# Kernel optimization log

Measured on AMD Instinct MI355X. Metric: run time of the kernel, lower is better.

The kernel has to match this reference:

```python
import jax, jax.numpy as jnp
import numpy as np

T, B, IN, H, OUT = 1024, 128, 6, 1536, 5


def setup_inputs() -> dict:
    key = jax.random.key(0)
    ks = jax.random.split(key, 11)
    s = 1.0 / np.sqrt(H)  # PyTorch cell init range
    u = lambda k, shape: jax.random.uniform(k, shape, jnp.float32, -s, s)
    return {
        "rnn_input": jax.random.normal(ks[0], (T, B, IN), jnp.float32),
        "W_ih0": u(ks[1], (4 * H, IN)),
        "W_hh0": u(ks[2], (4 * H, H)),
        "b_ih0": u(ks[3], (4 * H,)),
        "b_hh0": u(ks[4], (4 * H,)),
        "W_ih1": u(ks[5], (4 * H, H)),
        "W_hh1": u(ks[6], (4 * H, H)),
        "b_ih1": u(ks[7], (4 * H,)),
        "b_hh1": u(ks[8], (4 * H,)),
        "W_lin": u(ks[9], (OUT, H)),
        "b_lin": u(ks[10], (OUT,)),
    }


def _lstm_cell(x, h, c, W_ih, W_hh, b):
    # PyTorch LSTMCell: gates ordered (input, forget, cell, output)
    gates = x @ W_ih.T + h @ W_hh.T + b  # [B, 4H]
    i, f, g, o = jnp.split(gates, 4, axis=-1)
    c_new = jax.nn.sigmoid(f) * c + jax.nn.sigmoid(i) * jnp.tanh(g)
    h_new = jax.nn.sigmoid(o) * jnp.tanh(c_new)
    return h_new, c_new


def reference(rnn_input, W_ih0, W_hh0, b_ih0, b_hh0,
              W_ih1, W_hh1, b_ih1, b_hh1, W_lin, b_lin):
    b0 = b_ih0 + b_hh0
    b1 = b_ih1 + b_hh1
    batch = rnn_input.shape[1]
    h = rnn_input.dtype
    z = jnp.zeros((batch, H), h)

    def step(carry, x_t):
        h0, c0, h1, c1 = carry
        h0, c0 = _lstm_cell(x_t, h0, c0, W_ih0, W_hh0, b0)
        h1, c1 = _lstm_cell(h0, h1, c1, W_ih1, W_hh1, b1)
        return (h0, c0, h1, c1), None

    (h0, c0, h1, c1), _ = jax.lax.scan(step, (z, z, z, z), rnn_input)
    # Module's forward returns only the last-timestep linear output
    return h1 @ W_lin.T + b_lin  # [B, OUT]
```

## Files before the change

### kernel.cpp

```cpp
#include <hip/hip_runtime.h>

#define TSTEPS 1024
#define BATCH  128
#define HDIM   1536
#define NB_L0  96
#define NB_L1  128
#define NBLK   (NB_L0 + NB_L1)
#define K0P    1600
#define K1P    3072

typedef _Float16 f16x8 __attribute__((ext_vector_type(8)));
typedef float    f32x4 __attribute__((ext_vector_type(4)));

#define OFF_C0   0ul
#define OFF_C1   1024ul
#define OFF_H0   4096ul
#define OFF_H1   (OFF_H0 + 4ul*BATCH*HDIM*2)
#define OFF_WP0  (OFF_H1 + 2ul*BATCH*HDIM*2)
#define OFF_WP1  (OFF_WP0 + 96ul*64*K0P*2)
#define OFF_WLP  (OFF_WP1 + 128ul*48*K1P*2)
#define WS_NEED  (OFF_WLP + 16ul*HDIM*2)

#define SM_PARK  98304
#define SM_CST   147456
#define SM_BG    155648
#define SM_BYTES 155904

#define MFMA(a,b,c) __builtin_amdgcn_mfma_f32_16x16x32_f16(a,b,c,0,0,0)
#define LDSBAR()  asm volatile("s_waitcnt lgkmcnt(0)\n\ts_barrier" ::: "memory")
#define WAITVM8() asm volatile("s_waitcnt vmcnt(8)" ::: "memory")
#define WAITVM0() asm volatile("s_waitcnt vmcnt(0)" ::: "memory")

__device__ __forceinline__ float sgf(float x) { return 1.f/(1.f + __expf(-x)); }
__device__ __forceinline__ float thf(float x) { float e = __expf(2.f*x); return 1.f - 2.f/(e+1.f); }

__device__ __forceinline__ void gld16(const _Float16* g, char* lds) {
  __builtin_amdgcn_global_load_lds(
      (const __attribute__((address_space(1))) unsigned int*)g,
      (__attribute__((address_space(3))) unsigned int*)lds, 16, 0, 0);
}

__device__ __forceinline__ void group_bar(unsigned* lines, unsigned target, int tid) {
  __syncthreads();
  if (tid == 0)
    __hip_atomic_fetch_add(lines + (blockIdx.x & 7)*32, 1u,
                           __ATOMIC_RELEASE, __HIP_MEMORY_SCOPE_AGENT);
  if (tid < 8) {
    while (__hip_atomic_load(lines + tid*32, __ATOMIC_RELAXED,
                             __HIP_MEMORY_SCOPE_AGENT) < target)
      __builtin_amdgcn_s_sleep(1);
    __builtin_amdgcn_fence(__ATOMIC_ACQUIRE, "agent");
  }
  __syncthreads();
}

__device__ __forceinline__ void wait_group(unsigned* lines, unsigned target, int tid) {
  if (tid < 8) {
    while (__hip_atomic_load(lines + tid*32, __ATOMIC_RELAXED,
                             __HIP_MEMORY_SCOPE_AGENT) < target)
      __builtin_amdgcn_s_sleep(1);
    __builtin_amdgcn_fence(__ATOMIC_ACQUIRE, "agent");
  }
  __syncthreads();
}

__global__ void convert_weights(const float* __restrict__ Wih0, const float* __restrict__ Whh0,
                                const float* __restrict__ Wih1, const float* __restrict__ Whh1,
                                const float* __restrict__ Wlin,
                                _Float16* __restrict__ Wp0, _Float16* __restrict__ Wp1,
                                _Float16* __restrict__ Wlp) {
  const unsigned N0 = 96u*64u*K0P, N1 = 128u*48u*K1P, N2 = 16u*HDIM;
  const unsigned NT = N0 + N1 + N2;
  for (unsigned i = blockIdx.x*blockDim.x + threadIdx.x; i < NT; i += gridDim.x*blockDim.x) {
    if (i < N0) {
      unsigned blk = i / (64u*K0P), r = i - blk*64u*K0P;
      unsigned p = r / K0P, kk = r - p*K0P;
      unsigned srow = (p>>4)*HDIM + blk*16 + (p&15);
      float v;
      if (kk < 64u) v = (kk < 6u) ? Wih0[srow*6 + kk] : 0.f;
      else          v = Whh0[(size_t)srow*HDIM + (kk-64u)];
      Wp0[i] = (_Float16)v;
    } else if (i < N0 + N1) {
      unsigned ii = i - N0;
      unsigned blk = ii / (48u*K1P), r = ii - blk*48u*K1P;
      unsigned p = r / K1P, kk = r - p*K1P;
      unsigned srow = (p/12u)*HDIM + blk*12 + (p%12u);
      float v = (kk < (unsigned)HDIM) ? Wih1[(size_t)srow*HDIM + kk]
                                      : Whh1[(size_t)srow*HDIM + (kk-HDIM)];
      Wp1[ii] = (_Float16)v;
    } else {
      unsigned ii = i - N0 - N1;
      unsigned rr = ii / HDIM, k = ii - rr*HDIM;
      Wlp[ii] = (_Float16)(rr < 5 ? Wlin[rr*HDIM + k] : 0.f);
    }
  }
}

__global__ __launch_bounds__(256, 1) void lstm_persistent(
    const float* __restrict__ xall,
    const float* __restrict__ bih0, const float* __restrict__ bhh0,
    const float* __restrict__ bih1, const float* __restrict__ bhh1,
    const float* __restrict__ blin,
    const _Float16* __restrict__ Wp0, const _Float16* __restrict__ Wp1,
    const _Float16* __restrict__ Wlp,
    _Float16* __restrict__ h0b, _Float16* __restrict__ h1b,
    unsigned* __restrict__ c0l, unsigned* __restrict__ c1l,
    float* __restrict__ out)
{
  extern __shared__ __align__(16) char smem[];
  char*  park = smem + SM_PARK;
  float* cst  = (float*)(smem + SM_CST);
  float* bg   = (float*)(smem + SM_BG);
  float* gbuf = (float*)smem;

  const int tid = threadIdx.x, bid = blockIdx.x;
  const int wv = tid >> 6, lane = tid & 63, q = lane >> 4, l15 = lane & 15;
  const int BH = BATCH*HDIM;

  int dmaoff[8];
#pragma unroll
  for (int i = 0; i < 8; ++i) {
    int m = wv*32 + i*4 + (lane>>4), w16 = lane & 15;
    int u = (w16 & 8) | ((w16 ^ (m & 7)) & 7);
    dmaoff[i] = m*HDIM + u*8;
  }
  const int uA = wv*4 + q;
  int addrA[8];
#pragma unroll
  for (int mt = 0; mt < 8; ++mt) {
    int m = mt*16 + l15;
    int swz = (uA & 8) | ((uA ^ (m & 7)) & 7);
    addrA[mt] = m*256 + swz*16;
  }

  if (bid < NB_L0) {
    for (int p = tid; p < 64; p += 256) {
      int srow = (p>>4)*HDIM + (bid<<4) + (p&15);
      bg[p] = bih0[srow] + bhh0[srow];
    }
    for (int i = tid; i < BATCH*16; i += 256) cst[i] = 0.f;
    f16x8 bw[13][4];
#pragma unroll
    for (int wi = 0; wi < 13; ++wi)
#pragma unroll
      for (int nt = 0; nt < 4; ++nt)
        bw[wi][nt] = *(const f16x8*)(Wp0 + ((size_t)(bid*64 + nt*16 + l15))*K0P
                                         + (4*wi + wv)*32 + q*8);
    __syncthreads();

#pragma unroll 1
    for (int s = 0; s < TSTEPS; ++s) {
      if (s >= 4) wait_group(c1l, 16u*(unsigned)(s-3), tid);

      const _Float16* h0r = h0b + (size_t)((s+3)&3)*BH;
      _Float16*       h0w = h0b + (size_t)(s&3)*BH;
      const float*    xs  = xall + (size_t)s*BATCH*6;

#pragma unroll
      for (int i = 0; i < 8; ++i)
        gld16(h0r + 64 + dmaoff[i], smem + 32768 + (wv*8+i)*1024);
#pragma unroll
      for (int i = 0; i < 4; ++i) {
        int sidx = i*256 + tid, m = sidx>>3, w8 = sidx&7;
        int u = w8 ^ (m & 7);
        f16x8 v = {0,0,0,0,0,0,0,0};
        if (u == 0) {
#pragma unroll
          for (int j = 0; j < 6; ++j) v[j] = (_Float16)xs[m*6 + j];
        }
        *(f16x8*)(smem + m*256 + w8*16) = v;
      }
#pragma unroll
      for (int i = 0; i < 4; ++i) {
        int sidx = i*256 + tid, m = sidx>>3, w8 = sidx&7;
        int u8 = (w8 ^ (m & 7)) & 7;
        f16x8 hv = *(const f16x8*)(h0r + m*HDIM + u8*8);
        *(f16x8*)(smem + m*256 + (8 + w8)*16) = hv;
      }
      f32x4 acc[8][4];
#pragma unroll
      for (int mt = 0; mt < 8; ++mt)
#pragma unroll
        for (int nt = 0; nt < 4; ++nt) { f32x4 z = {0,0,0,0}; acc[mt][nt] = z; }

#pragma unroll
      for (int wi = 0; wi < 13; ++wi) {
        if (wi == 12)      WAITVM0();
        else if (wi >= 1)  WAITVM8();
        LDSBAR();
        if (wi + 2 < 13) {
          const _Float16* src = h0r + (wi+2)*128 - 64;
          char* dst = smem + ((wi+2)%3)*32768;
#pragma unroll
          for (int i = 0; i < 8; ++i) gld16(src + dmaoff[i], dst + (wv*8+i)*1024);
        }
        if (4*wi + wv < 50) {
          const char* bs = smem + (wi%3)*32768;
#pragma unroll
          for (int mt = 0; mt < 8; ++mt) {
            f16x8 a = *(const f16x8*)(bs + addrA[mt]);
#pragma unroll
            for (int nt = 0; nt < 4; ++nt)
              acc[mt][nt] = MFMA(a, bw[wi][nt], acc[mt][nt]);
          }
        }
      }
      LDSBAR();

#pragma unroll
      for (int r = 0; r < 4; ++r) {
        int nt = (wv + r) & 3;
#pragma unroll
        for (int mt = 0; mt < 8; ++mt) {
          f32x4 av = (nt==0)?acc[mt][0]:(nt==1)?acc[mt][1]:(nt==2)?acc[mt][2]:acc[mt][3];
          float* p = gbuf + (nt*16 + l15)*132 + (mt*16 + q*4);
          if (r == 0) *(f32x4*)p = av;
          else        { f32x4 o = *(const f32x4*)p; *(f32x4*)p = o + av; }
        }
        LDSBAR();
      }
#pragma unroll
      for (int e = 0; e < 8; ++e) {
        int idx = e*256 + tid, m = idx>>4, j = idx&15;
        float gi = gbuf[j*132 + m]        + bg[j];
        float gf = gbuf[(16+j)*132 + m]   + bg[16+j];
        float gg = gbuf[(32+j)*132 + m]   + bg[32+j];
        float go = gbuf[(48+j)*132 + m]   + bg[48+j];
        float co = cst[m*16 + j];
        float cn = sgf(gf)*co + sgf(gi)*thf(gg);
        cst[m*16 + j] = cn;
        h0w[(size_t)m*HDIM + (bid<<4) + j] = (_Float16)(sgf(go)*thf(cn));
      }
      group_bar(c0l, 12u*(unsigned)(s+1), tid);
    }
  } else {
    const int bid1 = bid - NB_L0;
    for (int p = tid; p < 48; p += 256) {
      int srow = (p/12)*HDIM + bid1*12 + (p%12);
      bg[p] = bih1[srow] + bhh1[srow];
    }
    for (int i = tid; i < 64*12; i += 256) cst[i] = 0.f;
    f16x8 bw1[20][3];
#pragma unroll
    for (int wi = 0; wi < 20; ++wi)
#pragma unroll
      for (int nt = 0; nt < 3; ++nt)
        bw1[wi][nt] = *(const f16x8*)(Wp1 + ((size_t)(bid1*48 + nt*16 + l15))*K1P
                                          + (4*wi + wv)*32 + q*8);
    for (int idx = tid; idx < 16*3*64; idx += 256) {
      int cl = idx/192, rem = idx - cl*192, nt = rem>>6, l = rem&63;
      f16x8 v = *(const f16x8*)(Wp1 + ((size_t)(bid1*48 + nt*16 + (l&15)))*K1P
                                    + (80 + cl)*32 + (l>>4)*8);
      *(f16x8*)(park + idx*16) = v;
    }
    __syncthreads();

#pragma unroll 1
    for (int s = 1; s <= TSTEPS; ++s) {
      wait_group(c0l, 12u*(unsigned)s, tid);

      const _Float16* h0r = h0b + (size_t)((s-1)&3)*BH;
      const _Float16* h1r = h1b + (size_t)(s&1)*BH;
      _Float16*       h1w = h1b + (size_t)((s-1)&1)*BH;

#pragma unroll
      for (int i = 0; i < 8; ++i) gld16(h0r +   0 + dmaoff[i], smem +     0 + (wv*8+i)*1024);
#pragma unroll
      for (int i = 0; i < 8; ++i) gld16(h0r + 128 + dmaoff[i], smem + 32768 + (wv*8+i)*1024);
      f32x4 acc[8][3];
#pragma unroll
      for (int mt = 0; mt < 8; ++mt)
#pragma unroll
        for (int nt = 0; nt < 3; ++nt) { f32x4 z = {0,0,0,0}; acc[mt][nt] = z; }

#pragma unroll
      for (int wi = 0; wi < 24; ++wi) {
        if (wi == 23) WAITVM0(); else WAITVM8();
        LDSBAR();
        if (wi + 2 < 24) {
          int wn = wi + 2;
          const _Float16* src = (wn < 12) ? (h0r + wn*128) : (h1r + (wn-12)*128);
          char* dst = smem + (wn%3)*32768;
#pragma unroll
          for (int i = 0; i < 8; ++i) gld16(src + dmaoff[i], dst + (wv*8+i)*1024);
        }
        const char* bs = smem + (wi%3)*32768;
        if (wi < 20) {
#pragma unroll
          for (int mt = 0; mt < 8; ++mt) {
            f16x8 a = *(const f16x8*)(bs + addrA[mt]);
#pragma unroll
            for (int nt = 0; nt < 3; ++nt)
              acc[mt][nt] = MFMA(a, bw1[wi][nt], acc[mt][nt]);
          }
        } else {
          f16x8 p0 = *(const f16x8*)(park + ((((wi-20)*4 + wv)*3 + 0)*64 + lane)*16);
          f16x8 p1 = *(const f16x8*)(park + ((((wi-20)*4 + wv)*3 + 1)*64 + lane)*16);
          f16x8 p2 = *(const f16x8*)(park + ((((wi-20)*4 + wv)*3 + 2)*64 + lane)*16);
#pragma unroll
          for (int mt = 0; mt < 8; ++mt) {
            f16x8 a = *(const f16x8*)(bs + addrA[mt]);
            acc[mt][0] = MFMA(a, p0, acc[mt][0]);
            acc[mt][1] = MFMA(a, p1, acc[mt][1]);
            acc[mt][2] = MFMA(a, p2, acc[mt][2]);
          }
        }
      }
      LDSBAR();

#pragma unroll
      for (int r = 0; r < 4; ++r) {
        int nt = (wv + r) & 3;
        if (nt < 3) {
#pragma unroll
          for (int mt = 0; mt < 8; ++mt) {
            f32x4 av = (nt==0)?acc[mt][0]:(nt==1)?acc[mt][1]:acc[mt][2];
            float* p = gbuf + (nt*16 + l15)*132 + (mt*16 + q*4);
            if (r == 0) *(f32x4*)p = av;
            else        { f32x4 o = *(const f32x4*)p; *(f32x4*)p = o + av; }
          }
        }
        LDSBAR();
      }
#pragma unroll
      for (int e = 0; e < 8; ++e) {
        int idx = e*256 + tid, m = idx>>4, j = idx&15;
        if (j < 12) {
          float gi = gbuf[j*132 + m]        + bg[j];
          float gf = gbuf[(12+j)*132 + m]   + bg[12+j];
          float gg = gbuf[(24+j)*132 + m]   + bg[24+j];
          float go = gbuf[(36+j)*132 + m]   + bg[36+j];
          float co = cst[m*12 + j];
          float cn = sgf(gf)*co + sgf(gi)*thf(gg);
          cst[m*12 + j] = cn;
          h1w[(size_t)m*HDIM + bid1*12 + j] = (_Float16)(sgf(go)*thf(cn));
        }
      }
      group_bar(c1l, 16u*(unsigned)s, tid);
    }

    if (bid == NB_L0) {
      const _Float16* h1r = h1b + (size_t)((TSTEPS-1)&1)*BH;
      f32x4 a8[8];
#pragma unroll
      for (int i = 0; i < 8; ++i) { f32x4 z = {0,0,0,0}; a8[i] = z; }
      for (int c = wv*12; c < wv*12 + 12; ++c) {
        f16x8 bf = *(const f16x8*)(Wlp + (size_t)l15*HDIM + c*32 + q*8);
#pragma unroll
        for (int mt = 0; mt < 8; ++mt) {
          f16x8 a = *(const f16x8*)(h1r + (size_t)(mt*16 + l15)*HDIM + c*32 + q*8);
          a8[mt] = MFMA(a, bf, a8[mt]);
        }
      }
      float* pl = (float*)smem;
#pragma unroll
      for (int mt = 0; mt < 8; ++mt)
#pragma unroll
        for (int rg = 0; rg < 4; ++rg)
          pl[wv*2048 + (mt*16 + q*4 + rg)*16 + l15] = a8[mt][rg];
      __syncthreads();
      for (int e = tid; e < 640; e += 256) {
        int b = e/5, o = e - 5*b;
        out[e] = blin[o] + pl[b*16+o] + pl[2048 + b*16+o] + pl[4096 + b*16+o] + pl[6144 + b*16+o];
      }
    }
  }
}

extern "C" void kernel_launch(void* const* d_in, const int* in_sizes, int n_in,
                              void* d_out, int out_size, void* d_ws, size_t ws_size,
                              hipStream_t stream) {
  (void)in_sizes; (void)n_in; (void)out_size;
  if (ws_size < WS_NEED) return;

  const float* x    = (const float*)d_in[0];
  const float* Wih0 = (const float*)d_in[1];
  const float* Whh0 = (const float*)d_in[2];
  const float* bih0 = (const float*)d_in[3];
  const float* bhh0 = (const float*)d_in[4];
  const float* Wih1 = (const float*)d_in[5];
  const float* Whh1 = (const float*)d_in[6];
  const float* bih1 = (const float*)d_in[7];
  const float* bhh1 = (const float*)d_in[8];
  const float* Wlin = (const float*)d_in[9];
  const float* blin = (const float*)d_in[10];

  char* ws = (char*)d_ws;
  unsigned*  c0l = (unsigned*)(ws + OFF_C0);
  unsigned*  c1l = (unsigned*)(ws + OFF_C1);
  _Float16*  h0b = (_Float16*)(ws + OFF_H0);
  _Float16*  h1b = (_Float16*)(ws + OFF_H1);
  _Float16*  Wp0 = (_Float16*)(ws + OFF_WP0);
  _Float16*  Wp1 = (_Float16*)(ws + OFF_WP1);
  _Float16*  Wlp = (_Float16*)(ws + OFF_WLP);
  float*     out = (float*)d_out;

  hipMemsetAsync(ws, 0, OFF_WP0, stream);
  hipLaunchKernelGGL(convert_weights, dim3(4096), dim3(256), 0, stream,
                     Wih0, Whh0, Wih1, Whh1, Wlin, Wp0, Wp1, Wlp);

  hipFuncSetAttribute((const void*)lstm_persistent,
                      hipFuncAttributeMaxDynamicSharedMemorySize, 160*1024);

  void* args[14];
  args[0]  = (void*)&x;    args[1]  = (void*)&bih0; args[2]  = (void*)&bhh0;
  args[3]  = (void*)&bih1; args[4]  = (void*)&bhh1; args[5]  = (void*)&blin;
  args[6]  = (void*)&Wp0;  args[7]  = (void*)&Wp1;  args[8]  = (void*)&Wlp;
  args[9]  = (void*)&h0b;  args[10] = (void*)&h1b;  args[11] = (void*)&c0l;
  args[12] = (void*)&c1l;  args[13] = (void*)&out;
  hipError_t err = hipLaunchCooperativeKernel((const void*)lstm_persistent,
                                              dim3(NBLK), dim3(256),
                                              args, (unsigned)SM_BYTES, stream);
  if (err != hipSuccess) {
    hipLaunchKernelGGL(lstm_persistent, dim3(NBLK), dim3(256), SM_BYTES, stream,
                       x, bih0, bhh0, bih1, bhh1, blin, Wp0, Wp1, Wlp,
                       h0b, h1b, c0l, c1l, out);
  }
}
```

Baseline: 28.05 ms.

## Give each layer-1 wave a private LDS ring to drop per-chunk block barriers

In the layer-1 blocks, each wave now DMA-loads only its own 32-column K slice of h into a private triple-buffered LDS ring. It uses a new swizzle and issues the next load after its own reads finish, so the block-wide s_barrier on every K chunk is gone. Waves then run the 24-chunk MFMA loop independently, synchronising only with vmcnt/lgkmcnt waits and sched barriers. The cost is a different LDS layout and smaller DMA batches per wave, and correctness now rests on the per-wave wait ordering.

```diff
diff --git a/kernel.cpp b/kernel.cpp
--- a/kernel.cpp
+++ b/kernel.cpp
@@ -28,8 +28,9 @@
 
 #define MFMA(a,b,c) __builtin_amdgcn_mfma_f32_16x16x32_f16(a,b,c,0,0,0)
 #define LDSBAR()  asm volatile("s_waitcnt lgkmcnt(0)\n\ts_barrier" ::: "memory")
-#define WAITVM8() asm volatile("s_waitcnt vmcnt(8)" ::: "memory")
-#define WAITVM0() asm volatile("s_waitcnt vmcnt(0)" ::: "memory")
+#define WAITVM(n) asm volatile("s_waitcnt vmcnt(" #n ")" ::: "memory")
+#define WAITLGKM() asm volatile("s_waitcnt lgkmcnt(0)" ::: "memory")
+#define SCHB()    __builtin_amdgcn_sched_barrier(0)
 
 __device__ __forceinline__ float sgf(float x) { return 1.f/(1.f + __expf(-x)); }
 __device__ __forceinline__ float thf(float x) { float e = __expf(2.f*x); return 1.f - 2.f/(e+1.f); }
@@ -108,7 +109,6 @@
     float* __restrict__ out)
 {
   extern __shared__ __align__(16) char smem[];
-  char*  park = smem + SM_PARK;
   float* cst  = (float*)(smem + SM_CST);
   float* bg   = (float*)(smem + SM_BG);
   float* gbuf = (float*)smem;
@@ -117,23 +117,23 @@
   const int wv = tid >> 6, lane = tid & 63, q = lane >> 4, l15 = lane & 15;
   const int BH = BATCH*HDIM;
 
-  int dmaoff[8];
-#pragma unroll
-  for (int i = 0; i < 8; ++i) {
-    int m = wv*32 + i*4 + (lane>>4), w16 = lane & 15;
-    int u = (w16 & 8) | ((w16 ^ (m & 7)) & 7);
-    dmaoff[i] = m*HDIM + u*8;
-  }
-  const int uA = wv*4 + q;
-  int addrA[8];
-#pragma unroll
-  for (int mt = 0; mt < 8; ++mt) {
-    int m = mt*16 + l15;
-    int swz = (uA & 8) | ((uA ^ (m & 7)) & 7);
-    addrA[mt] = m*256 + swz*16;
-  }
-
   if (bid < NB_L0) {
+    int dmaoff[8];
+#pragma unroll
+    for (int i = 0; i < 8; ++i) {
+      int m = wv*32 + i*4 + (lane>>4), w16 = lane & 15;
+      int u = (w16 & 8) | ((w16 ^ (m & 7)) & 7);
+      dmaoff[i] = m*HDIM + u*8;
+    }
+    const int uA = wv*4 + q;
+    int addrA[8];
+#pragma unroll
+    for (int mt = 0; mt < 8; ++mt) {
+      int m = mt*16 + l15;
+      int swz = (uA & 8) | ((uA ^ (m & 7)) & 7);
+      addrA[mt] = m*256 + swz*16;
+    }
+
     for (int p = tid; p < 64; p += 256) {
       int srow = (p>>4)*HDIM + (bid<<4) + (p&15);
       bg[p] = bih0[srow] + bhh0[srow];
@@ -185,8 +185,8 @@
 
 #pragma unroll
       for (int wi = 0; wi < 13; ++wi) {
-        if (wi == 12)      WAITVM0();
-        else if (wi >= 1)  WAITVM8();
+        if (wi == 12)      WAITVM(0);
+        else if (wi >= 1)  WAITVM(8);
         LDSBAR();
         if (wi + 2 < 13) {
           const _Float16* src = h0r + (wi+2)*128 - 64;
@@ -235,6 +235,15 @@
     }
   } else {
     const int bid1 = bid - NB_L0;
+    char* park = smem + SM_PARK;
+    char* const ring = smem + wv*24576;
+
+    int dmaoff2[8];
+#pragma unroll
+    for (int i = 0; i < 8; ++i)
+      dmaoff2[i] = (i*16 + (lane>>2))*HDIM + (((lane&3) ^ ((lane>>4)&3))<<3);
+    const int aOff = l15*64 + ((q ^ (l15>>2))<<4);
+
     for (int p = tid; p < 48; p += 256) {
       int srow = (p/12)*HDIM + bid1*12 + (p%12);
       bg[p] = bih1[srow] + bhh1[srow];
@@ -263,10 +272,15 @@
       const _Float16* h1r = h1b + (size_t)(s&1)*BH;
       _Float16*       h1w = h1b + (size_t)((s-1)&1)*BH;
 
-#pragma unroll
-      for (int i = 0; i < 8; ++i) gld16(h0r +   0 + dmaoff[i], smem +     0 + (wv*8+i)*1024);
-#pragma unroll
-      for (int i = 0; i < 8; ++i) gld16(h0r + 128 + dmaoff[i], smem + 32768 + (wv*8+i)*1024);
+      auto issue1 = [&](int wn) {
+        const _Float16* src = (wn < 12) ? (h0r + wn*128 + wv*32)
+                                        : (h1r + (wn-12)*128 + wv*32);
+        char* dst = ring + (wn%3)*8192;
+#pragma unroll
+        for (int i = 0; i < 8; ++i) gld16(src + dmaoff2[i], dst + i*1024);
+      };
+      issue1(0); issue1(1);
+
       f32x4 acc[8][3];
 #pragma unroll
       for (int mt = 0; mt < 8; ++mt)
@@ -275,36 +289,33 @@
 
 #pragma unroll
       for (int wi = 0; wi < 24; ++wi) {
-        if (wi == 23) WAITVM0(); else WAITVM8();
-        LDSBAR();
-        if (wi + 2 < 24) {
-          int wn = wi + 2;
-          const _Float16* src = (wn < 12) ? (h0r + wn*128) : (h1r + (wn-12)*128);
-          char* dst = smem + (wn%3)*32768;
-#pragma unroll
-          for (int i = 0; i < 8; ++i) gld16(src + dmaoff[i], dst + (wv*8+i)*1024);
-        }
-        const char* bs = smem + (wi%3)*32768;
+        if (wi == 23) WAITVM(0); else WAITVM(8);
+        SCHB();
+        const char* bs = ring + (wi%3)*8192;
         if (wi < 20) {
 #pragma unroll
           for (int mt = 0; mt < 8; ++mt) {
-            f16x8 a = *(const f16x8*)(bs + addrA[mt]);
-#pragma unroll
-            for (int nt = 0; nt < 3; ++nt)
-              acc[mt][nt] = MFMA(a, bw1[wi][nt], acc[mt][nt]);
+            f16x8 a = *(const f16x8*)(bs + mt*1024 + aOff);
+            acc[mt][0] = MFMA(a, bw1[wi][0], acc[mt][0]);
+            acc[mt][1] = MFMA(a, bw1[wi][1], acc[mt][1]);
+            acc[mt][2] = MFMA(a, bw1[wi][2], acc[mt][2]);
           }
         } else {
-          f16x8 p0 = *(const f16x8*)(park + ((((wi-20)*4 + wv)*3 + 0)*64 + lane)*16);
-          f16x8 p1 = *(const f16x8*)(park + ((((wi-20)*4 + wv)*3 + 1)*64 + lane)*16);
-          f16x8 p2 = *(const f16x8*)(park + ((((wi-20)*4 + wv)*3 + 2)*64 + lane)*16);
+          const int cl = (wi-20)*4 + wv;
+          f16x8 p0 = *(const f16x8*)(park + ((cl*3+0)*64 + lane)*16);
+          f16x8 p1 = *(const f16x8*)(park + ((cl*3+1)*64 + lane)*16);
+          f16x8 p2 = *(const f16x8*)(park + ((cl*3+2)*64 + lane)*16);
 #pragma unroll
           for (int mt = 0; mt < 8; ++mt) {
-            f16x8 a = *(const f16x8*)(bs + addrA[mt]);
+            f16x8 a = *(const f16x8*)(bs + mt*1024 + aOff);
             acc[mt][0] = MFMA(a, p0, acc[mt][0]);
             acc[mt][1] = MFMA(a, p1, acc[mt][1]);
             acc[mt][2] = MFMA(a, p2, acc[mt][2]);
           }
         }
+        WAITLGKM();
+        SCHB();
+        if (wi + 2 < 24) issue1(wi + 2);
       }
       LDSBAR();
 
```

Result: slower. 32.42 ms (+15.6%).

## Start layer-1 step with recurrent h1 chunks and defer layer-0 wait

Applied to the files above, without the earlier changes.

Layer-1 blocks now process the K dimension in rotated order: they first stream and multiply the h1 (own recurrent) chunks, and only wait on the layer-0 group barrier after ten chunks, before touching h0 data. The intent is to overlap the cross-layer dependency wait with useful MFMA work. The gate epilogues in both layers are also restructured so each thread handles several contiguous hidden units of one batch row, giving vectorized cell-state and h stores. The cst init bound for layer 1 is widened to cover all 128 batch rows.

```diff
diff --git a/kernel.cpp b/kernel.cpp
--- a/kernel.cpp
+++ b/kernel.cpp
@@ -10,7 +10,9 @@
 #define K1P    3072
 
 typedef _Float16 f16x8 __attribute__((ext_vector_type(8)));
+typedef _Float16 f16x2 __attribute__((ext_vector_type(2)));
 typedef float    f32x4 __attribute__((ext_vector_type(4)));
+typedef float    f32x2 __attribute__((ext_vector_type(2)));
 
 #define OFF_C0   0ul
 #define OFF_C1   1024ul
@@ -219,17 +221,26 @@
         }
         LDSBAR();
       }
-#pragma unroll
-      for (int e = 0; e < 8; ++e) {
-        int idx = e*256 + tid, m = idx>>4, j = idx&15;
-        float gi = gbuf[j*132 + m]        + bg[j];
-        float gf = gbuf[(16+j)*132 + m]   + bg[16+j];
-        float gg = gbuf[(32+j)*132 + m]   + bg[32+j];
-        float go = gbuf[(48+j)*132 + m]   + bg[48+j];
-        float co = cst[m*16 + j];
-        float cn = sgf(gf)*co + sgf(gi)*thf(gg);
-        cst[m*16 + j] = cn;
-        h0w[(size_t)m*HDIM + (bid<<4) + j] = (_Float16)(sgf(go)*thf(cn));
+      {
+        const int m = tid >> 1, jb = (tid & 1) * 8;
+        f32x4 cv0 = *(f32x4*)(cst + m*16 + jb);
+        f32x4 cv1 = *(f32x4*)(cst + m*16 + jb + 4);
+        f16x8 hv;
+#pragma unroll
+        for (int u = 0; u < 8; ++u) {
+          int j = jb + u;
+          float gi = gbuf[j*132 + m]        + bg[j];
+          float gf = gbuf[(16+j)*132 + m]   + bg[16+j];
+          float gg = gbuf[(32+j)*132 + m]   + bg[32+j];
+          float go = gbuf[(48+j)*132 + m]   + bg[48+j];
+          float co = (u < 4) ? cv0[u] : cv1[u-4];
+          float cn = sgf(gf)*co + sgf(gi)*thf(gg);
+          if (u < 4) cv0[u] = cn; else cv1[u-4] = cn;
+          hv[u] = (_Float16)(sgf(go)*thf(cn));
+        }
+        *(f32x4*)(cst + m*16 + jb)     = cv0;
+        *(f32x4*)(cst + m*16 + jb + 4) = cv1;
+        *(f16x8*)(h0w + (size_t)m*HDIM + (bid<<4) + jb) = hv;
       }
       group_bar(c0l, 12u*(unsigned)(s+1), tid);
     }
@@ -239,7 +250,7 @@
       int srow = (p/12)*HDIM + bid1*12 + (p%12);
       bg[p] = bih1[srow] + bhh1[srow];
     }
-    for (int i = tid; i < 64*12; i += 256) cst[i] = 0.f;
+    for (int i = tid; i < BATCH*12; i += 256) cst[i] = 0.f;
     f16x8 bw1[20][3];
 #pragma unroll
     for (int wi = 0; wi < 20; ++wi)
@@ -257,16 +268,14 @@
 
 #pragma unroll 1
     for (int s = 1; s <= TSTEPS; ++s) {
-      wait_group(c0l, 12u*(unsigned)s, tid);
-
       const _Float16* h0r = h0b + (size_t)((s-1)&3)*BH;
       const _Float16* h1r = h1b + (size_t)(s&1)*BH;
       _Float16*       h1w = h1b + (size_t)((s-1)&1)*BH;
 
 #pragma unroll
-      for (int i = 0; i < 8; ++i) gld16(h0r +   0 + dmaoff[i], smem +     0 + (wv*8+i)*1024);
-#pragma unroll
-      for (int i = 0; i < 8; ++i) gld16(h0r + 128 + dmaoff[i], smem + 32768 + (wv*8+i)*1024);
+      for (int i = 0; i < 8; ++i) gld16(h1r +   0 + dmaoff[i], smem +     0 + (wv*8+i)*1024);
+#pragma unroll
+      for (int i = 0; i < 8; ++i) gld16(h1r + 128 + dmaoff[i], smem + 32768 + (wv*8+i)*1024);
       f32x4 acc[8][3];
 #pragma unroll
       for (int mt = 0; mt < 8; ++mt)
@@ -274,29 +283,32 @@
         for (int nt = 0; nt < 3; ++nt) { f32x4 z = {0,0,0,0}; acc[mt][nt] = z; }
 
 #pragma unroll
-      for (int wi = 0; wi < 24; ++wi) {
-        if (wi == 23) WAITVM0(); else WAITVM8();
+      for (int k = 0; k < 24; ++k) {
+        if (k == 10) wait_group(c0l, 12u*(unsigned)s, tid);
+        if (k == 23) WAITVM0(); else WAITVM8();
         LDSBAR();
-        if (wi + 2 < 24) {
-          int wn = wi + 2;
+        if (k + 2 < 24) {
+          int wn = (k + 14) % 24;
           const _Float16* src = (wn < 12) ? (h0r + wn*128) : (h1r + (wn-12)*128);
-          char* dst = smem + (wn%3)*32768;
+          char* dst = smem + ((k+2)%3)*32768;
 #pragma unroll
           for (int i = 0; i < 8; ++i) gld16(src + dmaoff[i], dst + (wv*8+i)*1024);
         }
-        const char* bs = smem + (wi%3)*32768;
-        if (wi < 20) {
+        const char* bs = smem + (k%3)*32768;
+        const int p = (k + 12) % 24;
+        if (p < 20) {
 #pragma unroll
           for (int mt = 0; mt < 8; ++mt) {
             f16x8 a = *(const f16x8*)(bs + addrA[mt]);
 #pragma unroll
             for (int nt = 0; nt < 3; ++nt)
-              acc[mt][nt] = MFMA(a, bw1[wi][nt], acc[mt][nt]);
+              acc[mt][nt] = MFMA(a, bw1[p][nt], acc[mt][nt]);
           }
         } else {
-          f16x8 p0 = *(const f16x8*)(park + ((((wi-20)*4 + wv)*3 + 0)*64 + lane)*16);
-          f16x8 p1 = *(const f16x8*)(park + ((((wi-20)*4 + wv)*3 + 1)*64 + lane)*16);
-          f16x8 p2 = *(const f16x8*)(park + ((((wi-20)*4 + wv)*3 + 2)*64 + lane)*16);
+          const int cl = (p-20)*4 + wv;
+          f16x8 p0 = *(const f16x8*)(park + ((cl*3+0)*64 + lane)*16);
+          f16x8 p1 = *(const f16x8*)(park + ((cl*3+1)*64 + lane)*16);
+          f16x8 p2 = *(const f16x8*)(park + ((cl*3+2)*64 + lane)*16);
 #pragma unroll
           for (int mt = 0; mt < 8; ++mt) {
             f16x8 a = *(const f16x8*)(bs + addrA[mt]);
@@ -322,18 +334,28 @@
         }
         LDSBAR();
       }
-#pragma unroll
-      for (int e = 0; e < 8; ++e) {
-        int idx = e*256 + tid, m = idx>>4, j = idx&15;
-        if (j < 12) {
+      {
+        const int m = tid >> 1, jb = (tid & 1) * 6;
+        f32x2 cv[3];
+#pragma unroll
+        for (int v = 0; v < 3; ++v) cv[v] = *(f32x2*)(cst + m*12 + jb + 2*v);
+        f16x2 hv[3];
+#pragma unroll
+        for (int u = 0; u < 6; ++u) {
+          int j = jb + u;
           float gi = gbuf[j*132 + m]        + bg[j];
           float gf = gbuf[(12+j)*132 + m]   + bg[12+j];
           float gg = gbuf[(24+j)*132 + m]   + bg[24+j];
           float go = gbuf[(36+j)*132 + m]   + bg[36+j];
-          float co = cst[m*12 + j];
+          float co = cv[u>>1][u&1];
           float cn = sgf(gf)*co + sgf(gi)*thf(gg);
-          cst[m*12 + j] = cn;
-          h1w[(size_t)m*HDIM + bid1*12 + j] = (_Float16)(sgf(go)*thf(cn));
+          cv[u>>1][u&1] = cn;
+          hv[u>>1][u&1] = (_Float16)(sgf(go)*thf(cn));
+        }
+#pragma unroll
+        for (int v = 0; v < 3; ++v) {
+          *(f32x2*)(cst + m*12 + jb + 2*v) = cv[v];
+          *(f16x2*)(h1w + (size_t)m*HDIM + bid1*12 + jb + 2*v) = hv[v];
         }
       }
       group_bar(c1l, 16u*(unsigned)s, tid);
```

Result: slower. 30.11 ms (+7.3%).

## Split layer-1 GEMM into K-halves across block pairs with partial-sum exchange

Applied to the files above, without the earlier changes.

Layer-1 blocks are paired: each pair shares a 24-unit output tile, one block multiplies by W_ih1 against h0 and the other by W_hh1 against h1. Each block handles half of the batch rows for the gate nonlinearity and swaps partial sums with its partner through global memory and a flag handshake. The h1-side block no longer waits for layer 0 before starting its GEMM, which is meant to shorten the per-step critical path. The cost is an extra global round-trip and spin-wait between partners every step, plus more accumulator registers (8x6 tiles).

```diff
diff --git a/kernel.cpp b/kernel.cpp
--- a/kernel.cpp
+++ b/kernel.cpp
@@ -7,10 +7,11 @@
 #define NB_L1  128
 #define NBLK   (NB_L0 + NB_L1)
 #define K0P    1600
-#define K1P    3072
+#define K1H    1536
 
 typedef _Float16 f16x8 __attribute__((ext_vector_type(8)));
 typedef float    f32x4 __attribute__((ext_vector_type(4)));
+typedef float    f32x2 __attribute__((ext_vector_type(2)));
 
 #define OFF_C0   0ul
 #define OFF_C1   1024ul
@@ -18,13 +19,15 @@
 #define OFF_H1   (OFF_H0 + 4ul*BATCH*HDIM*2)
 #define OFF_WP0  (OFF_H1 + 2ul*BATCH*HDIM*2)
 #define OFF_WP1  (OFF_WP0 + 96ul*64*K0P*2)
-#define OFF_WLP  (OFF_WP1 + 128ul*48*K1P*2)
-#define WS_NEED  (OFF_WLP + 16ul*HDIM*2)
+#define OFF_WLP  (OFF_WP1 + 128ul*96*K1H*2)
+#define OFF_PART (OFF_WLP + 16ul*HDIM*2)
+#define OFF_PFLG (OFF_PART + 128ul*64*96*4)
+#define WS_NEED  (OFF_PFLG + 128ul*128)
 
 #define SM_PARK  98304
 #define SM_CST   147456
 #define SM_BG    155648
-#define SM_BYTES 155904
+#define SM_BYTES 156160
 
 #define MFMA(a,b,c) __builtin_amdgcn_mfma_f32_16x16x32_f16(a,b,c,0,0,0)
 #define LDSBAR()  asm volatile("s_waitcnt lgkmcnt(0)\n\ts_barrier" ::: "memory")
@@ -69,7 +72,7 @@
                                 const float* __restrict__ Wlin,
                                 _Float16* __restrict__ Wp0, _Float16* __restrict__ Wp1,
                                 _Float16* __restrict__ Wlp) {
-  const unsigned N0 = 96u*64u*K0P, N1 = 128u*48u*K1P, N2 = 16u*HDIM;
+  const unsigned N0 = 96u*64u*K0P, N1 = 128u*96u*K1H, N2 = 16u*HDIM;
   const unsigned NT = N0 + N1 + N2;
   for (unsigned i = blockIdx.x*blockDim.x + threadIdx.x; i < NT; i += gridDim.x*blockDim.x) {
     if (i < N0) {
@@ -82,11 +85,11 @@
       Wp0[i] = (_Float16)v;
     } else if (i < N0 + N1) {
       unsigned ii = i - N0;
-      unsigned blk = ii / (48u*K1P), r = ii - blk*48u*K1P;
-      unsigned p = r / K1P, kk = r - p*K1P;
-      unsigned srow = (p/12u)*HDIM + blk*12 + (p%12u);
-      float v = (kk < (unsigned)HDIM) ? Wih1[(size_t)srow*HDIM + kk]
-                                      : Whh1[(size_t)srow*HDIM + (kk-HDIM)];
+      unsigned blk = ii / (96u*K1H), r = ii - blk*96u*K1H;
+      unsigned p = r / K1H, kk = r - p*K1H;
+      unsigned ntile = blk >> 1, kt = blk & 1;
+      unsigned srow = (p/24u)*HDIM + ntile*24u + (p%24u);
+      float v = kt ? Whh1[(size_t)srow*HDIM + kk] : Wih1[(size_t)srow*HDIM + kk];
       Wp1[ii] = (_Float16)v;
     } else {
       unsigned ii = i - N0 - N1;
@@ -105,7 +108,7 @@
     const _Float16* __restrict__ Wlp,
     _Float16* __restrict__ h0b, _Float16* __restrict__ h1b,
     unsigned* __restrict__ c0l, unsigned* __restrict__ c1l,
-    float* __restrict__ out)
+    float* __restrict__ out, float* __restrict__ part, unsigned* __restrict__ pflg)
 {
   extern __shared__ __align__(16) char smem[];
   char*  park = smem + SM_PARK;
@@ -235,105 +238,148 @@
     }
   } else {
     const int bid1 = bid - NB_L0;
-    for (int p = tid; p < 48; p += 256) {
-      int srow = (p/12)*HDIM + bid1*12 + (p%12);
+    const int ntile = bid1 >> 1, kt = bid1 & 1;
+    const int mybase = kt * 64, otherbase = (1 - kt) * 64;
+    float*       partMy = part + (size_t)bid1 * 6144;
+    const float* partPn = part + (size_t)(bid1 ^ 1) * 6144;
+    unsigned*    flgMy  = pflg + bid1 * 32;
+    unsigned*    flgPn  = pflg + (bid1 ^ 1) * 32;
+    float*       pbuf   = (float*)(smem + 65536);
+
+    for (int p = tid; p < 96; p += 256) {
+      int srow = (p/24)*HDIM + ntile*24 + (p%24);
       bg[p] = bih1[srow] + bhh1[srow];
     }
-    for (int i = tid; i < 64*12; i += 256) cst[i] = 0.f;
-    f16x8 bw1[20][3];
-#pragma unroll
-    for (int wi = 0; wi < 20; ++wi)
-#pragma unroll
-      for (int nt = 0; nt < 3; ++nt)
-        bw1[wi][nt] = *(const f16x8*)(Wp1 + ((size_t)(bid1*48 + nt*16 + l15))*K1P
+    for (int i = tid; i < 64*24; i += 256) cst[i] = 0.f;
+    f16x8 bw1[10][6];
+#pragma unroll
+    for (int wi = 0; wi < 10; ++wi)
+#pragma unroll
+      for (int nt = 0; nt < 6; ++nt)
+        bw1[wi][nt] = *(const f16x8*)(Wp1 + ((size_t)(bid1*96 + nt*16 + l15))*K1H
                                           + (4*wi + wv)*32 + q*8);
-    for (int idx = tid; idx < 16*3*64; idx += 256) {
-      int cl = idx/192, rem = idx - cl*192, nt = rem>>6, l = rem&63;
-      f16x8 v = *(const f16x8*)(Wp1 + ((size_t)(bid1*48 + nt*16 + (l&15)))*K1P
-                                    + (80 + cl)*32 + (l>>4)*8);
+    for (int idx = tid; idx < 8*6*64; idx += 256) {
+      int cl = idx/384, rem = idx - cl*384, nt = rem>>6, l = rem&63;
+      f16x8 v = *(const f16x8*)(Wp1 + ((size_t)(bid1*96 + nt*16 + (l&15)))*K1H
+                                    + ((10 + (cl>>2))*4 + (cl&3))*32 + (l>>4)*8);
       *(f16x8*)(park + idx*16) = v;
     }
     __syncthreads();
 
 #pragma unroll 1
     for (int s = 1; s <= TSTEPS; ++s) {
-      wait_group(c0l, 12u*(unsigned)s, tid);
-
       const _Float16* h0r = h0b + (size_t)((s-1)&3)*BH;
       const _Float16* h1r = h1b + (size_t)(s&1)*BH;
       _Float16*       h1w = h1b + (size_t)((s-1)&1)*BH;
 
-#pragma unroll
-      for (int i = 0; i < 8; ++i) gld16(h0r +   0 + dmaoff[i], smem +     0 + (wv*8+i)*1024);
-#pragma unroll
-      for (int i = 0; i < 8; ++i) gld16(h0r + 128 + dmaoff[i], smem + 32768 + (wv*8+i)*1024);
-      f32x4 acc[8][3];
+      if (kt == 0) wait_group(c0l, 12u*(unsigned)s, tid);
+      const _Float16* kb = kt ? h1r : h0r;
+
+#pragma unroll
+      for (int i = 0; i < 8; ++i) gld16(kb +   0 + dmaoff[i], smem +     0 + (wv*8+i)*1024);
+#pragma unroll
+      for (int i = 0; i < 8; ++i) gld16(kb + 128 + dmaoff[i], smem + 32768 + (wv*8+i)*1024);
+      f32x4 acc[8][6];
 #pragma unroll
       for (int mt = 0; mt < 8; ++mt)
 #pragma unroll
-        for (int nt = 0; nt < 3; ++nt) { f32x4 z = {0,0,0,0}; acc[mt][nt] = z; }
-
-#pragma unroll
-      for (int wi = 0; wi < 24; ++wi) {
-        if (wi == 23) WAITVM0(); else WAITVM8();
+        for (int nt = 0; nt < 6; ++nt) { f32x4 z = {0,0,0,0}; acc[mt][nt] = z; }
+
+#pragma unroll
+      for (int wi = 0; wi < 12; ++wi) {
+        if (wi == 11) WAITVM0(); else WAITVM8();
         LDSBAR();
-        if (wi + 2 < 24) {
-          int wn = wi + 2;
-          const _Float16* src = (wn < 12) ? (h0r + wn*128) : (h1r + (wn-12)*128);
-          char* dst = smem + (wn%3)*32768;
+        if (wi + 2 < 12) {
+          const _Float16* src = kb + (wi+2)*128;
+          char* dst = smem + ((wi+2)%3)*32768;
 #pragma unroll
           for (int i = 0; i < 8; ++i) gld16(src + dmaoff[i], dst + (wv*8+i)*1024);
         }
         const char* bs = smem + (wi%3)*32768;
-        if (wi < 20) {
+        if (wi < 10) {
 #pragma unroll
           for (int mt = 0; mt < 8; ++mt) {
             f16x8 a = *(const f16x8*)(bs + addrA[mt]);
 #pragma unroll
-            for (int nt = 0; nt < 3; ++nt)
+            for (int nt = 0; nt < 6; ++nt)
               acc[mt][nt] = MFMA(a, bw1[wi][nt], acc[mt][nt]);
           }
         } else {
-          f16x8 p0 = *(const f16x8*)(park + ((((wi-20)*4 + wv)*3 + 0)*64 + lane)*16);
-          f16x8 p1 = *(const f16x8*)(park + ((((wi-20)*4 + wv)*3 + 1)*64 + lane)*16);
-          f16x8 p2 = *(const f16x8*)(park + ((((wi-20)*4 + wv)*3 + 2)*64 + lane)*16);
+          const int cl = (wi-10)*4 + wv;
+          f16x8 p0 = *(const f16x8*)(park + ((cl*6+0)*64 + lane)*16);
+          f16x8 p1 = *(const f16x8*)(park + ((cl*6+1)*64 + lane)*16);
+          f16x8 p2 = *(const f16x8*)(park + ((cl*6+2)*64 + lane)*16);
+          f16x8 p3 = *(const f16x8*)(park + ((cl*6+3)*64 + lane)*16);
+          f16x8 p4 = *(const f16x8*)(park + ((cl*6+4)*64 + lane)*16);
+          f16x8 p5 = *(const f16x8*)(park + ((cl*6+5)*64 + lane)*16);
 #pragma unroll
           for (int mt = 0; mt < 8; ++mt) {
             f16x8 a = *(const f16x8*)(bs + addrA[mt]);
             acc[mt][0] = MFMA(a, p0, acc[mt][0]);
             acc[mt][1] = MFMA(a, p1, acc[mt][1]);
             acc[mt][2] = MFMA(a, p2, acc[mt][2]);
+            acc[mt][3] = MFMA(a, p3, acc[mt][3]);
+            acc[mt][4] = MFMA(a, p4, acc[mt][4]);
+            acc[mt][5] = MFMA(a, p5, acc[mt][5]);
           }
         }
       }
       LDSBAR();
 
 #pragma unroll
-      for (int r = 0; r < 4; ++r) {
-        int nt = (wv + r) & 3;
-        if (nt < 3) {
-#pragma unroll
-          for (int mt = 0; mt < 8; ++mt) {
-            f32x4 av = (nt==0)?acc[mt][0]:(nt==1)?acc[mt][1]:acc[mt][2];
-            float* p = gbuf + (nt*16 + l15)*132 + (mt*16 + q*4);
-            if (r == 0) *(f32x4*)p = av;
-            else        { f32x4 o = *(const f32x4*)p; *(f32x4*)p = o + av; }
-          }
+      for (int r = 0; r < 6; ++r) {
+        int nt = wv + r; if (nt >= 6) nt -= 6;
+        bool first = (r == ((nt < 4) ? 0 : nt - 3));
+#pragma unroll
+        for (int mt = 0; mt < 8; ++mt) {
+          f32x4 av = (nt==0)?acc[mt][0]:(nt==1)?acc[mt][1]:(nt==2)?acc[mt][2]
+                   :(nt==3)?acc[mt][3]:(nt==4)?acc[mt][4]:acc[mt][5];
+          float* p = gbuf + (nt*16 + l15)*132 + (mt*16 + q*4);
+          if (first) *(f32x4*)p = av;
+          else       { f32x4 o = *(const f32x4*)p; *(f32x4*)p = o + av; }
         }
         LDSBAR();
       }
-#pragma unroll
-      for (int e = 0; e < 8; ++e) {
-        int idx = e*256 + tid, m = idx>>4, j = idx&15;
-        if (j < 12) {
-          float gi = gbuf[j*132 + m]        + bg[j];
-          float gf = gbuf[(12+j)*132 + m]   + bg[12+j];
-          float gg = gbuf[(24+j)*132 + m]   + bg[24+j];
-          float go = gbuf[(36+j)*132 + m]   + bg[36+j];
-          float co = cst[m*12 + j];
+
+      {
+        const int mb2 = tid >> 2, gseg = (tid & 3) * 24;
+        const int mo = otherbase + mb2;
+#pragma unroll
+        for (int t = 0; t < 24; t += 2) {
+          f32x2 v;
+          v[0] = gbuf[(gseg+t  )*132 + mo];
+          v[1] = gbuf[(gseg+t+1)*132 + mo];
+          *(f32x2*)(partMy + mb2*96 + gseg + t) = v;
+        }
+      }
+      __syncthreads();
+      if (tid == 0) {
+        __hip_atomic_store(flgMy, (unsigned)s, __ATOMIC_RELEASE, __HIP_MEMORY_SCOPE_AGENT);
+        while (__hip_atomic_load(flgPn, __ATOMIC_RELAXED, __HIP_MEMORY_SCOPE_AGENT) < (unsigned)s)
+          __builtin_amdgcn_s_sleep(1);
+        __builtin_amdgcn_fence(__ATOMIC_ACQUIRE, "agent");
+      }
+      __syncthreads();
+
+      for (int e = 0; e < 6; ++e) {
+        int idx = (e*256 + tid)*4;
+        *(f32x4*)(pbuf + idx) = *(const f32x4*)(partPn + idx);
+      }
+      __syncthreads();
+      {
+        const int mb = tid >> 2, jb = (tid & 3) * 6;
+        const int m = mybase + mb;
+#pragma unroll
+        for (int u = 0; u < 6; ++u) {
+          int j = jb + u;
+          float gi = gbuf[j*132 + m]       + pbuf[mb*96 + j]      + bg[j];
+          float gf = gbuf[(24+j)*132 + m]  + pbuf[mb*96 + 24+j]   + bg[24+j];
+          float gg = gbuf[(48+j)*132 + m]  + pbuf[mb*96 + 48+j]   + bg[48+j];
+          float go = gbuf[(72+j)*132 + m]  + pbuf[mb*96 + 72+j]   + bg[72+j];
+          float co = cst[mb*24 + j];
           float cn = sgf(gf)*co + sgf(gi)*thf(gg);
-          cst[m*12 + j] = cn;
-          h1w[(size_t)m*HDIM + bid1*12 + j] = (_Float16)(sgf(go)*thf(cn));
+          cst[mb*24 + j] = cn;
+          h1w[(size_t)m*HDIM + ntile*24 + j] = (_Float16)(sgf(go)*thf(cn));
         }
       }
       group_bar(c1l, 16u*(unsigned)s, tid);
@@ -386,34 +432,38 @@
   const float* blin = (const float*)d_in[10];
 
   char* ws = (char*)d_ws;
-  unsigned*  c0l = (unsigned*)(ws + OFF_C0);
-  unsigned*  c1l = (unsigned*)(ws + OFF_C1);
-  _Float16*  h0b = (_Float16*)(ws + OFF_H0);
-  _Float16*  h1b = (_Float16*)(ws + OFF_H1);
-  _Float16*  Wp0 = (_Float16*)(ws + OFF_WP0);
-  _Float16*  Wp1 = (_Float16*)(ws + OFF_WP1);
-  _Float16*  Wlp = (_Float16*)(ws + OFF_WLP);
-  float*     out = (float*)d_out;
+  unsigned*  c0l  = (unsigned*)(ws + OFF_C0);
+  unsigned*  c1l  = (unsigned*)(ws + OFF_C1);
+  _Float16*  h0b  = (_Float16*)(ws + OFF_H0);
+  _Float16*  h1b  = (_Float16*)(ws + OFF_H1);
+  _Float16*  Wp0  = (_Float16*)(ws + OFF_WP0);
+  _Float16*  Wp1  = (_Float16*)(ws + OFF_WP1);
+  _Float16*  Wlp  = (_Float16*)(ws + OFF_WLP);
+  float*     part = (float*)(ws + OFF_PART);
+  unsigned*  pflg = (unsigned*)(ws + OFF_PFLG);
+  float*     out  = (float*)d_out;
 
   hipMemsetAsync(ws, 0, OFF_WP0, stream);
+  hipMemsetAsync(ws + OFF_PFLG, 0, 128*128, stream);
   hipLaunchKernelGGL(convert_weights, dim3(4096), dim3(256), 0, stream,
                      Wih0, Whh0, Wih1, Whh1, Wlin, Wp0, Wp1, Wlp);
 
   hipFuncSetAttribute((const void*)lstm_persistent,
                       hipFuncAttributeMaxDynamicSharedMemorySize, 160*1024);
 
-  void* args[14];
+  void* args[16];
   args[0]  = (void*)&x;    args[1]  = (void*)&bih0; args[2]  = (void*)&bhh0;
   args[3]  = (void*)&bih1; args[4]  = (void*)&bhh1; args[5]  = (void*)&blin;
   args[6]  = (void*)&Wp0;  args[7]  = (void*)&Wp1;  args[8]  = (void*)&Wlp;
   args[9]  = (void*)&h0b;  args[10] = (void*)&h1b;  args[11] = (void*)&c0l;
-  args[12] = (void*)&c1l;  args[13] = (void*)&out;
+  args[12] = (void*)&c1l;  args[13] = (void*)&out;  args[14] = (void*)&part;
+  args[15] = (void*)&pflg;
   hipError_t err = hipLaunchCooperativeKernel((const void*)lstm_persistent,
                                               dim3(NBLK), dim3(256),
                                               args, (unsigned)SM_BYTES, stream);
   if (err != hipSuccess) {
     hipLaunchKernelGGL(lstm_persistent, dim3(NBLK), dim3(256), SM_BYTES, stream,
                        x, bih0, bhh0, bih1, bhh1, blin, Wp0, Wp1, Wlp,
-                       h0b, h1b, c0l, c1l, out);
-  }
-}
+                       h0b, h1b, c0l, c1l, out, part, pflg);
+  }
+}
```

New measurement: 45.98 ms. 1.64x slower.
